# Kernel tuning notes

Measured on AMD Instinct MI355X. Metric: run time of the kernel, lower is better.

Reference implementation:

```python
import jax, jax.numpy as jnp
import numpy as np

N_NODES = 10000
N_EDGES = 64000
N_GRAPHS = 64
HID = 64


def _nnconv(h, src, dst, edge_attr, w1, b1, w2, b2, root, bias):
    # edge MLP: Linear(dim_edge,64) -> ReLU -> Linear(64, 64*64)
    we = (jax.nn.relu(edge_attr @ w1 + b1) @ w2 + b2).reshape(-1, HID, HID)  # [E,64,64]
    # per-edge matmul of gathered source features, then scatter-add to dst
    msg = jnp.einsum('ei,eio->eo', h[src], we)                               # [E,64]
    agg = jax.ops.segment_sum(msg, dst, num_segments=N_NODES)               # [N,64]
    return agg + h @ root + bias


def setup_inputs() -> dict:
    key = jax.random.key(0)
    ks = jax.random.split(key, 20)
    s = 0.05
    inp = {
        'x': jax.random.normal(ks[0], (N_NODES, 128), jnp.float32),
        'edge_index': jax.random.randint(ks[1], (2, N_EDGES), 0, N_NODES, dtype=jnp.int64),
        'edge_attr': jax.random.normal(ks[2], (N_EDGES, 32), jnp.float32),
        'batch': jnp.sort(jax.random.randint(ks[3], (N_NODES,), 0, N_GRAPHS, dtype=jnp.int64)),
        'nfc_w': jax.random.normal(ks[4], (128, HID), jnp.float32) * s,
        'nfc_b': jnp.zeros((HID,), jnp.float32),
        'efc1_w1': jax.random.normal(ks[5], (32, HID), jnp.float32) * s,
        'efc1_b1': jnp.zeros((HID,), jnp.float32),
        'efc1_w2': jax.random.normal(ks[6], (HID, HID * HID), jnp.float32) * s,
        'efc1_b2': jnp.zeros((HID * HID,), jnp.float32),
        'gc1_root': jax.random.normal(ks[7], (HID, HID), jnp.float32) * s,
        'gc1_bias': jnp.zeros((HID,), jnp.float32),
        'efc2_w1': jax.random.normal(ks[8], (32, HID), jnp.float32) * s,
        'efc2_b1': jnp.zeros((HID,), jnp.float32),
        'efc2_w2': jax.random.normal(ks[9], (HID, HID * HID), jnp.float32) * s,
        'efc2_b2': jnp.zeros((HID * HID,), jnp.float32),
        'gc2_root': jax.random.normal(ks[10], (HID, HID), jnp.float32) * s,
        'gc2_bias': jnp.zeros((HID,), jnp.float32),
        'fc1_w': jax.random.normal(ks[11], (HID, 32), jnp.float32) * s,
        'fc1_b': jnp.zeros((32,), jnp.float32),
        'fc2_w': jax.random.normal(ks[12], (32, 1), jnp.float32) * s,
        'fc2_b': jnp.zeros((1,), jnp.float32),
    }
    return inp


def reference(x, edge_index, edge_attr, batch,
              nfc_w, nfc_b,
              efc1_w1, efc1_b1, efc1_w2, efc1_b2, gc1_root, gc1_bias,
              efc2_w1, efc2_b1, efc2_w2, efc2_b2, gc2_root, gc2_bias,
              fc1_w, fc1_b, fc2_w, fc2_b):
    lrelu = lambda v: jax.nn.leaky_relu(v, 0.01)
    src, dst = edge_index[0], edge_index[1]
    hx = lrelu(x @ nfc_w + nfc_b)
    hx = lrelu(_nnconv(hx, src, dst, edge_attr, efc1_w1, efc1_b1, efc1_w2, efc1_b2, gc1_root, gc1_bias))
    hx = lrelu(_nnconv(hx, src, dst, edge_attr, efc2_w1, efc2_b1, efc2_w2, efc2_b2, gc2_root, gc2_bias))
    hg = jax.ops.segment_sum(hx, batch, num_segments=N_GRAPHS)  # global_add_pool -> [G,64]
    hg = lrelu(hg @ fc1_w + fc1_b)
    return hg @ fc2_w + fc2_b
```

## Files before the change

### kernel.cpp

```cpp
#include <hip/hip_runtime.h>
#include <hip/hip_bf16.h>

#define N_NODES  10000
#define N_EDGES  64000
#define N_GRAPHS 64
#define HID      64

typedef __attribute__((ext_vector_type(8))) short short8;
typedef __attribute__((ext_vector_type(4))) float f32x4;

__device__ __forceinline__ float lrelu(float v){ return v > 0.f ? v : 0.01f*v; }

__device__ __forceinline__ unsigned short f2bf(float f){
    union { float f; unsigned u; } v; v.f = f;
    unsigned r = v.u + 0x7fff + ((v.u >> 16) & 1);
    return (unsigned short)(r >> 16);
}
__device__ __forceinline__ float bf2f(unsigned short s){
    union { unsigned u; float f; } v; v.u = ((unsigned)s) << 16;
    return v.f;
}

#define PRE_NFC 2500
#define PRE_W2C 128
#define PRE_TR  4
#define PRE_CNT 250
__global__ void __launch_bounds__(256) pre_kernel(
        const float* __restrict__ x, const float* __restrict__ nfc_w, const float* __restrict__ nfc_b,
        float* __restrict__ hx1,
        const float* __restrict__ e1w2, unsigned short* __restrict__ w2t1,
        const float* __restrict__ e2w2, unsigned short* __restrict__ w2t2,
        const float* __restrict__ e1w1, unsigned short* __restrict__ w1t1,
        const float* __restrict__ e2w1, unsigned short* __restrict__ w1t2,
        const float* __restrict__ e1b2, unsigned short* __restrict__ b2t1,
        const float* __restrict__ e2b2, unsigned short* __restrict__ b2t2,
        const int* __restrict__ src, int* __restrict__ counts){
    __shared__ float tile[64][65];
    int b = blockIdx.x, tid = threadIdx.x;
    if (b < PRE_NFC){
        int m = tid & 63, n = b * 4 + (tid >> 6);
        float acc = nfc_b[m];
        const float* row = x + (size_t)n * 128;
        #pragma unroll 8
        for (int k = 0; k < 128; ++k) acc += row[k] * nfc_w[k * 64 + m];
        hx1[(size_t)n * 64 + m] = lrelu(acc);
    } else if (b < PRE_NFC + PRE_W2C){
        int bb = b - PRE_NFC;
        int k = bb & 63;
        const float* srcw = ((bb < 64) ? e1w2 : e2w2) + (size_t)k * 4096;
        unsigned short* dstw = (bb < 64) ? w2t1 : w2t2;
        for (int idx = tid; idx < 4096; idx += 256) tile[idx >> 6][idx & 63] = srcw[idx];
        __syncthreads();
        for (int idx = tid; idx < 4096; idx += 256){
            int o = idx >> 6, i = idx & 63;
            dstw[((size_t)(k * 64 + o) << 6) + i] = f2bf(tile[i][o]);
        }
    } else if (b < PRE_NFC + PRE_W2C + PRE_TR){
        int bb = b - PRE_NFC - PRE_W2C;
        if (bb < 2){
            const float* w1 = bb ? e2w1 : e1w1;
            unsigned short* w1t = bb ? w1t2 : w1t1;
            for (int idx = tid; idx < 2048; idx += 256){
                int o = idx >> 5, k = idx & 31;
                w1t[idx] = f2bf(w1[k * 64 + o]);
            }
        } else {
            const float* b2 = (bb == 3) ? e2b2 : e1b2;
            unsigned short* b2t = (bb == 3) ? b2t2 : b2t1;
            for (int idx = tid; idx < 4096; idx += 256){
                int o = idx >> 6, i = idx & 63;
                b2t[idx] = f2bf(b2[i * 64 + o]);
            }
        }
    } else {
        int e = (b - PRE_NFC - PRE_W2C - PRE_TR) * 256 + tid;
        if (e < N_EDGES) atomicAdd(&counts[src[e]], 1);
    }
}

__global__ void csr_scan_kernel(const int* __restrict__ counts, int* __restrict__ rowptr,
                                int* __restrict__ cursor){
    __shared__ int part[256];
    int tid = threadIdx.x;
    const int CH = (N_NODES + 255) / 256;
    int base = tid * CH, s = 0;
    for (int i = 0; i < CH; ++i){ int idx = base + i; if (idx < N_NODES){ cursor[idx] = 0; s += counts[idx]; } }
    part[tid] = s; __syncthreads();
    for (int off = 1; off < 256; off <<= 1){
        int v = (tid >= off) ? part[tid - off] : 0;
        __syncthreads();
        part[tid] += v;
        __syncthreads();
    }
    int run = part[tid] - s;
    for (int i = 0; i < CH; ++i){ int idx = base + i; if (idx < N_NODES){ rowptr[idx] = run; run += counts[idx]; } }
    if (tid == 255) rowptr[N_NODES] = run;
}

__global__ void csr_scatter_kernel(const int* __restrict__ src, const int* __restrict__ dst,
                                   const int* __restrict__ rowptr, int* __restrict__ cursor,
                                   int* __restrict__ eidx, int* __restrict__ dsts){
    int e = blockIdx.x * 256 + threadIdx.x;
    if (e >= N_EDGES) return;
    int s = src[e];
    int j = rowptr[s] + atomicAdd(&cursor[s], 1);
    eidx[j] = e; dsts[j] = dst[e];
}

#define NBT2 1000
#define NBH2 157
#define NBG  (157 * 8)
template<int L2FLAG>
__global__ void __launch_bounds__(256) layerA_kernel(
        const float* __restrict__ ea, const int* __restrict__ eidx,
        const unsigned short* __restrict__ w1t, const float* __restrict__ b1,
        unsigned short* __restrict__ tp,
        const float* __restrict__ hx, const unsigned short* __restrict__ b2t,
        float* __restrict__ hb2, float* __restrict__ agg,
        const unsigned short* __restrict__ w2t, unsigned short* __restrict__ G,
        float* __restrict__ hg){
    __shared__ unsigned short stg[64 * 256];
    int b = blockIdx.x, tid = threadIdx.x;
    int wid = tid >> 6, l = tid & 63;
    int m16 = l & 15, grp = l >> 4;

    if (b < NBT2){
        int j = b * 64 + wid * 16 + m16;
        const float* row = ea + (size_t)eidx[j] * 32 + grp * 8;
        float4 f0 = *(const float4*)(row);
        float4 f1 = *(const float4*)(row + 4);
        short8 ef;
        ef[0]=(short)f2bf(f0.x); ef[1]=(short)f2bf(f0.y); ef[2]=(short)f2bf(f0.z); ef[3]=(short)f2bf(f0.w);
        ef[4]=(short)f2bf(f1.x); ef[5]=(short)f2bf(f1.y); ef[6]=(short)f2bf(f1.z); ef[7]=(short)f2bf(f1.w);
        #pragma unroll
        for (int TB = 0; TB < 64; TB += 16){
            short8 wf = *(const short8*)(w1t + (TB + m16) * 32 + grp * 8);
            f32x4 acc = *(const f32x4*)(b1 + TB + grp * 4);
            acc = __builtin_amdgcn_mfma_f32_16x16x32_bf16(wf, ef, acc, 0, 0, 0);
            unsigned p0 = (unsigned)f2bf(fmaxf(acc[0], 0.f)) | ((unsigned)f2bf(fmaxf(acc[1], 0.f)) << 16);
            unsigned p1 = (unsigned)f2bf(fmaxf(acc[2], 0.f)) | ((unsigned)f2bf(fmaxf(acc[3], 0.f)) << 16);
            uint2 pk; pk.x = p0; pk.y = p1;
            *(uint2*)(tp + ((size_t)j << 6) + TB + grp * 4) = pk;
        }
    } else if (b < NBT2 + NBH2){
        int bb = b - NBT2;
        int node = bb * 64 + wid * 16 + m16;
        short8 h0 = {0,0,0,0,0,0,0,0}, h1 = {0,0,0,0,0,0,0,0};
        if (node < N_NODES){
            const float* hp = hx + ((size_t)node << 6) + grp * 8;
            float4 f0 = *(const float4*)(hp);
            float4 f1 = *(const float4*)(hp + 4);
            float4 f2 = *(const float4*)(hp + 32);
            float4 f3 = *(const float4*)(hp + 36);
            h0[0]=(short)f2bf(f0.x); h0[1]=(short)f2bf(f0.y); h0[2]=(short)f2bf(f0.z); h0[3]=(short)f2bf(f0.w);
            h0[4]=(short)f2bf(f1.x); h0[5]=(short)f2bf(f1.y); h0[6]=(short)f2bf(f1.z); h0[7]=(short)f2bf(f1.w);
            h1[0]=(short)f2bf(f2.x); h1[1]=(short)f2bf(f2.y); h1[2]=(short)f2bf(f2.z); h1[3]=(short)f2bf(f2.w);
            h1[4]=(short)f2bf(f3.x); h1[5]=(short)f2bf(f3.y); h1[6]=(short)f2bf(f3.z); h1[7]=(short)f2bf(f3.w);
        }
        #pragma unroll
        for (int TB = 0; TB < 64; TB += 16){
            short8 c0 = *(const short8*)(b2t + (TB + m16) * 64 + grp * 8);
            short8 c1 = *(const short8*)(b2t + (TB + m16) * 64 + 32 + grp * 8);
            f32x4 acc = {0.f, 0.f, 0.f, 0.f};
            acc = __builtin_amdgcn_mfma_f32_16x16x32_bf16(c0, h0, acc, 0, 0, 0);
            acc = __builtin_amdgcn_mfma_f32_16x16x32_bf16(c1, h1, acc, 0, 0, 0);
            if (node < N_NODES) *(f32x4*)(hb2 + ((size_t)node << 6) + TB + grp * 4) = acc;
        }
        f32x4 z = {0.f, 0.f, 0.f, 0.f};
        #pragma unroll
        for (int q = 0; q < 4; ++q){
            int chunk = q * 256 + tid;
            int n = bb * 64 + (chunk >> 4), c = (chunk & 15) * 4;
            if (n < N_NODES) *(f32x4*)(agg + ((size_t)n << 6) + c) = z;
        }
    } else if (b < NBT2 + NBH2 + NBG){
        int g = b - NBT2 - NBH2;
        int bx = g >> 3, by = g & 7;
        int n0 = bx * 64;
        int cb = by * 512;

        short8 bf0[4], bf1[4];
        #pragma unroll
        for (int ng = 0; ng < 4; ++ng){
            int node = n0 + ng * 16 + m16;
            short8 b0 = {0,0,0,0,0,0,0,0}, b1v = {0,0,0,0,0,0,0,0};
            if (node < N_NODES){
                const float* hp = hx + ((size_t)node << 6) + grp * 8;
                float4 f0 = *(const float4*)(hp);
                float4 f1 = *(const float4*)(hp + 4);
                float4 f2 = *(const float4*)(hp + 32);
                float4 f3 = *(const float4*)(hp + 36);
                b0[0]=(short)f2bf(f0.x); b0[1]=(short)f2bf(f0.y); b0[2]=(short)f2bf(f0.z); b0[3]=(short)f2bf(f0.w);
                b0[4]=(short)f2bf(f1.x); b0[5]=(short)f2bf(f1.y); b0[6]=(short)f2bf(f1.z); b0[7]=(short)f2bf(f1.w);
                b1v[0]=(short)f2bf(f2.x); b1v[1]=(short)f2bf(f2.y); b1v[2]=(short)f2bf(f2.z); b1v[3]=(short)f2bf(f2.w);
                b1v[4]=(short)f2bf(f3.x); b1v[5]=(short)f2bf(f3.y); b1v[6]=(short)f2bf(f3.z); b1v[7]=(short)f2bf(f3.w);
            }
            bf0[ng] = b0; bf1[ng] = b1v;
        }

        for (int h = 0; h < 2; ++h){
            #pragma unroll
            for (int tt = 0; tt < 4; ++tt){
                int t = h * 4 + tt;
                int TB = cb + t * 64 + wid * 16;
                const unsigned short* ap = w2t + ((size_t)(TB + m16) << 6) + grp * 8;
                short8 a0 = *(const short8*)ap;
                short8 a1 = *(const short8*)(ap + 32);
                int inrow = (tt * 128 + wid * 32 + grp * 8) ^ ((m16 & 7) << 4);
                #pragma unroll
                for (int ng = 0; ng < 4; ++ng){
                    f32x4 acc = {0.f, 0.f, 0.f, 0.f};
                    acc = __builtin_amdgcn_mfma_f32_16x16x32_bf16(a0, bf0[ng], acc, 0, 0, 0);
                    acc = __builtin_amdgcn_mfma_f32_16x16x32_bf16(a1, bf1[ng], acc, 0, 0, 0);
                    unsigned p0 = (unsigned)f2bf(acc[0]) | ((unsigned)f2bf(acc[1]) << 16);
                    unsigned p1 = (unsigned)f2bf(acc[2]) | ((unsigned)f2bf(acc[3]) << 16);
                    int row = ng * 16 + m16;
                    uint2 pk; pk.x = p0; pk.y = p1;
                    *(uint2*)((char*)stg + row * 512 + inrow) = pk;
                }
            }
            __syncthreads();
            #pragma unroll
            for (int s = 0; s < 8; ++s){
                int ci = s * 256 + tid;
                int row = ci >> 5;
                int node = n0 + row;
                uint4 v = *(uint4*)((char*)stg + row * 512 + (((ci & 31) * 16) ^ ((row & 7) << 4)));
                if (node < N_NODES)
                    *(uint4*)(G + ((size_t)node << 12) + cb + h * 256 + (ci & 31) * 8) = v;
            }
            __syncthreads();
        }
    } else if (L2FLAG){
        for (int i = tid; i < N_GRAPHS * 64; i += 256) hg[i] = 0.f;
    }
}

__global__ void __launch_bounds__(64) msg_csr_kernel(
        const unsigned short* __restrict__ tp, const unsigned short* __restrict__ G,
        const float* __restrict__ hb2, const int* __restrict__ rowptr,
        const int* __restrict__ dsts, float* __restrict__ agg){
    int s = blockIdx.x;
    int o = threadIdx.x;
    __shared__ unsigned short gl[4096];
    __shared__ unsigned short ts[64] __attribute__((aligned(16)));
    int r0 = rowptr[s], r1 = rowptr[s + 1];
    if (r0 == r1) return;
    const short8* gsrc = (const short8*)(G + ((size_t)s << 12));
    short8* gld = (short8*)gl;
    #pragma unroll
    for (int i = 0; i < 8; ++i) gld[i * 64 + o] = gsrc[i * 64 + o];
    float g[64];
    #pragma unroll
    for (int k = 0; k < 64; ++k) g[k] = bf2f(gl[k * 64 + o]);
    float hb = hb2[((size_t)s << 6) + o];
    for (int j = r0; j < r1; ++j){
        ts[o] = tp[((size_t)j << 6) + o];
        float acc = hb;
        #pragma unroll
        for (int k8 = 0; k8 < 8; ++k8){
            short8 tv = *(const short8*)&ts[k8 * 8];
            #pragma unroll
            for (int u = 0; u < 8; ++u) acc += bf2f((unsigned short)tv[u]) * g[k8 * 8 + u];
        }
        atomicAdd(&agg[((size_t)dsts[j] << 6) + o], acc);
    }
}

__global__ void combine_kernel(const float* __restrict__ agg, const float* __restrict__ hx,
                               const float* __restrict__ root, const float* __restrict__ bias,
                               float* __restrict__ out, int N){
    int m = threadIdx.x;
    int n = blockIdx.x * 4 + threadIdx.y;
    if (n >= N) return;
    float acc = agg[(size_t)n * 64 + m] + bias[m];
    const float* row = hx + (size_t)n * 64;
    #pragma unroll 8
    for (int k = 0; k < 64; ++k) acc += row[k] * root[k * 64 + m];
    out[(size_t)n * 64 + m] = lrelu(acc);
}

__global__ void combine2_kernel(const float* __restrict__ agg, const float* __restrict__ hx,
                                const float* __restrict__ root, const float* __restrict__ bias,
                                const int* __restrict__ batch, float* __restrict__ hg, int N){
    int m = threadIdx.x;
    int n = blockIdx.x * 4 + threadIdx.y;
    if (n >= N) return;
    float acc = agg[(size_t)n * 64 + m] + bias[m];
    const float* row = hx + (size_t)n * 64;
    #pragma unroll 8
    for (int k = 0; k < 64; ++k) acc += row[k] * root[k * 64 + m];
    atomicAdd(&hg[batch[n] * 64 + m], lrelu(acc));
}

__global__ void head_kernel(const float* __restrict__ hg, const float* __restrict__ fc1w,
                            const float* __restrict__ fc1b, const float* __restrict__ fc2w,
                            const float* __restrict__ fc2b, float* __restrict__ out){
    int g = threadIdx.x;
    const float* row = hg + g * 64;
    float h1[32];
    #pragma unroll
    for (int j = 0; j < 32; ++j){
        float a = fc1b[j];
        #pragma unroll 8
        for (int i = 0; i < 64; ++i) a += row[i] * fc1w[i * 32 + j];
        h1[j] = lrelu(a);
    }
    float o = fc2b[0];
    #pragma unroll
    for (int j = 0; j < 32; ++j) o += h1[j] * fc2w[j];
    out[g] = o;
}

extern "C" void kernel_launch(void* const* d_in, const int* in_sizes, int n_in,
                              void* d_out, int out_size, void* d_ws, size_t ws_size,
                              hipStream_t stream){
    const float* x      = (const float*)d_in[0];
    const int*   ei     = (const int*)  d_in[1];
    const float* ea     = (const float*)d_in[2];
    const int*   batch  = (const int*)  d_in[3];
    const float* nfc_w  = (const float*)d_in[4];
    const float* nfc_b  = (const float*)d_in[5];
    const float* e1w1   = (const float*)d_in[6];
    const float* e1b1   = (const float*)d_in[7];
    const float* e1w2   = (const float*)d_in[8];
    const float* e1b2   = (const float*)d_in[9];
    const float* g1root = (const float*)d_in[10];
    const float* g1bias = (const float*)d_in[11];
    const float* e2w1   = (const float*)d_in[12];
    const float* e2b1   = (const float*)d_in[13];
    const float* e2w2   = (const float*)d_in[14];
    const float* e2b2   = (const float*)d_in[15];
    const float* g2root = (const float*)d_in[16];
    const float* g2bias = (const float*)d_in[17];
    const float* fc1w   = (const float*)d_in[18];
    const float* fc1b   = (const float*)d_in[19];
    const float* fc2w   = (const float*)d_in[20];
    const float* fc2b   = (const float*)d_in[21];
    float* out = (float*)d_out;

    const int* src = ei;
    const int* dst = ei + N_EDGES;

    char* ws = (char*)d_ws;
    float* hx1 = (float*)ws;               ws += (size_t)N_NODES * 64 * 4;
    float* hx2 = (float*)ws;               ws += (size_t)N_NODES * 64 * 4;
    unsigned short* tp = (unsigned short*)ws; ws += (size_t)N_EDGES * 64 * 2;
    float* hb2 = (float*)ws;               ws += (size_t)N_NODES * 64 * 4;
    float* agg = (float*)ws;               ws += (size_t)N_NODES * 64 * 4;
    float* hg  = (float*)ws;               ws += (size_t)N_GRAPHS * 64 * 4;
    unsigned short* w2t1 = (unsigned short*)ws; ws += (size_t)64 * 64 * 64 * 2;
    unsigned short* w2t2 = (unsigned short*)ws; ws += (size_t)64 * 64 * 64 * 2;
    unsigned short* w1t1 = (unsigned short*)ws; ws += (size_t)2048 * 2;
    unsigned short* w1t2 = (unsigned short*)ws; ws += (size_t)2048 * 2;
    unsigned short* b2t1 = (unsigned short*)ws; ws += (size_t)4096 * 2;
    unsigned short* b2t2 = (unsigned short*)ws; ws += (size_t)4096 * 2;
    int* counts = (int*)ws;                ws += (size_t)10240 * 4;
    int* cursor = (int*)ws;                ws += (size_t)10240 * 4;
    int* rowptr = (int*)ws;                ws += (size_t)10240 * 4;
    int* eidx   = (int*)ws;                ws += (size_t)N_EDGES * 4;
    int* dsts   = (int*)ws;                ws += (size_t)N_EDGES * 4;
    unsigned short* G = (unsigned short*)ws;

    dim3 blk(64, 4);

    hipMemsetAsync(counts, 0, (size_t)N_NODES * 4, stream);
    pre_kernel<<<PRE_NFC + PRE_W2C + PRE_TR + PRE_CNT, 256, 0, stream>>>(
        x, nfc_w, nfc_b, hx1, e1w2, w2t1, e2w2, w2t2,
        e1w1, w1t1, e2w1, w1t2, e1b2, b2t1, e2b2, b2t2, src, counts);
    csr_scan_kernel<<<1, 256, 0, stream>>>(counts, rowptr, cursor);
    csr_scatter_kernel<<<N_EDGES / 256, 256, 0, stream>>>(src, dst, rowptr, cursor, eidx, dsts);

    layerA_kernel<0><<<NBT2 + NBH2 + NBG, 256, 0, stream>>>(
        ea, eidx, w1t1, e1b1, tp, hx1, b2t1, hb2, agg, w2t1, G, nullptr);
    msg_csr_kernel<<<N_NODES, 64, 0, stream>>>(tp, G, hb2, rowptr, dsts, agg);
    combine_kernel<<<N_NODES / 4, blk, 0, stream>>>(agg, hx1, g1root, g1bias, hx2, N_NODES);

    layerA_kernel<1><<<NBT2 + NBH2 + NBG + 1, 256, 0, stream>>>(
        ea, eidx, w1t2, e2b1, tp, hx2, b2t2, hb2, agg, w2t2, G, hg);
    msg_csr_kernel<<<N_NODES, 64, 0, stream>>>(tp, G, hb2, rowptr, dsts, agg);
    combine2_kernel<<<N_NODES / 4, blk, 0, stream>>>(agg, hx2, g2root, g2bias, batch, hg, N_NODES);

    head_kernel<<<1, 64, 0, stream>>>(hg, fc1w, fc1b, fc2w, fc2b, out);
}
```

Baseline: 254.2 us.

## Move edge-MLP first layer to pre-kernel and use MFMA for node linears

Both layers' edge MLP hidden activations (tp1, tp2) are now computed in the pre-kernel, in original edge order, from a single load of edge_attr. msg_csr reaches them through eidx. The input node linear and both root-combine linears now run on bf16 MFMA using pre-transposed bf16 weights produced by a new init kernel, which also replaces the memset. This aims to take the tp computation off the per-layer critical path and to cut scalar FMA work, at the cost of an extra tp buffer, an indirect gather in msg_csr, and bf16 rounding in the node and root matmuls.

```diff
diff --git a/kernel.cpp b/kernel.cpp
--- a/kernel.cpp
+++ b/kernel.cpp
@@ -20,32 +20,119 @@
     union { unsigned u; float f; } v; v.u = ((unsigned)s) << 16;
     return v.f;
 }
-
-#define PRE_NFC 2500
-#define PRE_W2C 128
-#define PRE_TR  4
-#define PRE_CNT 250
-__global__ void __launch_bounds__(256) pre_kernel(
-        const float* __restrict__ x, const float* __restrict__ nfc_w, const float* __restrict__ nfc_b,
-        float* __restrict__ hx1,
-        const float* __restrict__ e1w2, unsigned short* __restrict__ w2t1,
-        const float* __restrict__ e2w2, unsigned short* __restrict__ w2t2,
+__device__ __forceinline__ short8 pack_bf8(float4 a, float4 b){
+    short8 r;
+    r[0]=(short)f2bf(a.x); r[1]=(short)f2bf(a.y); r[2]=(short)f2bf(a.z); r[3]=(short)f2bf(a.w);
+    r[4]=(short)f2bf(b.x); r[5]=(short)f2bf(b.y); r[6]=(short)f2bf(b.z); r[7]=(short)f2bf(b.w);
+    return r;
+}
+
+__global__ void __launch_bounds__(256) init_kernel(
+        int* __restrict__ counts,
+        const float* __restrict__ nfc_w, unsigned short* __restrict__ nfc_wt,
         const float* __restrict__ e1w1, unsigned short* __restrict__ w1t1,
         const float* __restrict__ e2w1, unsigned short* __restrict__ w1t2,
         const float* __restrict__ e1b2, unsigned short* __restrict__ b2t1,
         const float* __restrict__ e2b2, unsigned short* __restrict__ b2t2,
+        const float* __restrict__ g1root, unsigned short* __restrict__ rootT1,
+        const float* __restrict__ g2root, unsigned short* __restrict__ rootT2){
+    int b = blockIdx.x, tid = threadIdx.x;
+    if (b < 40){
+        int i = b * 256 + tid;
+        if (i < N_NODES) counts[i] = 0;
+    } else if (b == 40){
+        for (int idx = tid; idx < 8192; idx += 256){
+            int o = idx >> 7, i = idx & 127;
+            nfc_wt[idx] = f2bf(nfc_w[i * 64 + o]);
+        }
+    } else if (b <= 42){
+        const float* w1 = (b == 42) ? e2w1 : e1w1;
+        unsigned short* w1t = (b == 42) ? w1t2 : w1t1;
+        for (int idx = tid; idx < 2048; idx += 256){
+            int o = idx >> 5, k = idx & 31;
+            w1t[idx] = f2bf(w1[k * 64 + o]);
+        }
+    } else if (b <= 44){
+        const float* b2 = (b == 44) ? e2b2 : e1b2;
+        unsigned short* b2t = (b == 44) ? b2t2 : b2t1;
+        for (int idx = tid; idx < 4096; idx += 256){
+            int o = idx >> 6, i = idx & 63;
+            b2t[idx] = f2bf(b2[i * 64 + o]);
+        }
+    } else {
+        const float* rt = (b == 46) ? g2root : g1root;
+        unsigned short* rT = (b == 46) ? rootT2 : rootT1;
+        for (int idx = tid; idx < 4096; idx += 256){
+            int o = idx >> 6, i = idx & 63;
+            rT[idx] = f2bf(rt[i * 64 + o]);
+        }
+    }
+}
+
+#define PRE_NFC 157
+#define PRE_TG  1000
+#define PRE_W2C 128
+#define PRE_CNT 250
+__global__ void __launch_bounds__(256) pre_kernel(
+        const float* __restrict__ x, const unsigned short* __restrict__ nfc_wt,
+        const float* __restrict__ nfc_b, float* __restrict__ hx1,
+        const float* __restrict__ ea,
+        const unsigned short* __restrict__ w1t1, const float* __restrict__ e1b1, unsigned short* __restrict__ tp1,
+        const unsigned short* __restrict__ w1t2, const float* __restrict__ e2b1, unsigned short* __restrict__ tp2,
+        const float* __restrict__ e1w2, unsigned short* __restrict__ w2t1,
+        const float* __restrict__ e2w2, unsigned short* __restrict__ w2t2,
         const int* __restrict__ src, int* __restrict__ counts){
     __shared__ float tile[64][65];
     int b = blockIdx.x, tid = threadIdx.x;
+    int wid = tid >> 6, l = tid & 63;
+    int m16 = l & 15, grp = l >> 4;
     if (b < PRE_NFC){
-        int m = tid & 63, n = b * 4 + (tid >> 6);
-        float acc = nfc_b[m];
-        const float* row = x + (size_t)n * 128;
-        #pragma unroll 8
-        for (int k = 0; k < 128; ++k) acc += row[k] * nfc_w[k * 64 + m];
-        hx1[(size_t)n * 64 + m] = lrelu(acc);
-    } else if (b < PRE_NFC + PRE_W2C){
-        int bb = b - PRE_NFC;
+        int node = b * 64 + wid * 16 + m16;
+        bool ok = node < N_NODES;
+        short8 xb[4];
+        #pragma unroll
+        for (int kq = 0; kq < 4; ++kq){
+            if (ok){
+                const float* xp = x + (size_t)node * 128 + kq * 32 + grp * 8;
+                xb[kq] = pack_bf8(*(const float4*)xp, *(const float4*)(xp + 4));
+            } else {
+                short8 z = {0,0,0,0,0,0,0,0}; xb[kq] = z;
+            }
+        }
+        #pragma unroll
+        for (int TB = 0; TB < 64; TB += 16){
+            f32x4 acc = *(const f32x4*)(nfc_b + TB + grp * 4);
+            #pragma unroll
+            for (int kq = 0; kq < 4; ++kq){
+                short8 af = *(const short8*)(nfc_wt + (TB + m16) * 128 + kq * 32 + grp * 8);
+                acc = __builtin_amdgcn_mfma_f32_16x16x32_bf16(af, xb[kq], acc, 0, 0, 0);
+            }
+            f32x4 r;
+            r[0] = lrelu(acc[0]); r[1] = lrelu(acc[1]); r[2] = lrelu(acc[2]); r[3] = lrelu(acc[3]);
+            if (ok) *(f32x4*)(hx1 + ((size_t)node << 6) + TB + grp * 4) = r;
+        }
+    } else if (b < PRE_NFC + PRE_TG){
+        int j = (b - PRE_NFC) * 64 + wid * 16 + m16;
+        const float* row = ea + (size_t)j * 32 + grp * 8;
+        short8 ef = pack_bf8(*(const float4*)row, *(const float4*)(row + 4));
+        #pragma unroll
+        for (int TB = 0; TB < 64; TB += 16){
+            short8 wf1 = *(const short8*)(w1t1 + (TB + m16) * 32 + grp * 8);
+            f32x4 a1 = *(const f32x4*)(e1b1 + TB + grp * 4);
+            a1 = __builtin_amdgcn_mfma_f32_16x16x32_bf16(wf1, ef, a1, 0, 0, 0);
+            uint2 p;
+            p.x = (unsigned)f2bf(fmaxf(a1[0], 0.f)) | ((unsigned)f2bf(fmaxf(a1[1], 0.f)) << 16);
+            p.y = (unsigned)f2bf(fmaxf(a1[2], 0.f)) | ((unsigned)f2bf(fmaxf(a1[3], 0.f)) << 16);
+            *(uint2*)(tp1 + ((size_t)j << 6) + TB + grp * 4) = p;
+            short8 wf2 = *(const short8*)(w1t2 + (TB + m16) * 32 + grp * 8);
+            f32x4 a2 = *(const f32x4*)(e2b1 + TB + grp * 4);
+            a2 = __builtin_amdgcn_mfma_f32_16x16x32_bf16(wf2, ef, a2, 0, 0, 0);
+            p.x = (unsigned)f2bf(fmaxf(a2[0], 0.f)) | ((unsigned)f2bf(fmaxf(a2[1], 0.f)) << 16);
+            p.y = (unsigned)f2bf(fmaxf(a2[2], 0.f)) | ((unsigned)f2bf(fmaxf(a2[3], 0.f)) << 16);
+            *(uint2*)(tp2 + ((size_t)j << 6) + TB + grp * 4) = p;
+        }
+    } else if (b < PRE_NFC + PRE_TG + PRE_W2C){
+        int bb = b - PRE_NFC - PRE_TG;
         int k = bb & 63;
         const float* srcw = ((bb < 64) ? e1w2 : e2w2) + (size_t)k * 4096;
         unsigned short* dstw = (bb < 64) ? w2t1 : w2t2;
@@ -55,25 +142,8 @@
             int o = idx >> 6, i = idx & 63;
             dstw[((size_t)(k * 64 + o) << 6) + i] = f2bf(tile[i][o]);
         }
-    } else if (b < PRE_NFC + PRE_W2C + PRE_TR){
-        int bb = b - PRE_NFC - PRE_W2C;
-        if (bb < 2){
-            const float* w1 = bb ? e2w1 : e1w1;
-            unsigned short* w1t = bb ? w1t2 : w1t1;
-            for (int idx = tid; idx < 2048; idx += 256){
-                int o = idx >> 5, k = idx & 31;
-                w1t[idx] = f2bf(w1[k * 64 + o]);
-            }
-        } else {
-            const float* b2 = (bb == 3) ? e2b2 : e1b2;
-            unsigned short* b2t = (bb == 3) ? b2t2 : b2t1;
-            for (int idx = tid; idx < 4096; idx += 256){
-                int o = idx >> 6, i = idx & 63;
-                b2t[idx] = f2bf(b2[i * 64 + o]);
-            }
-        }
     } else {
-        int e = (b - PRE_NFC - PRE_W2C - PRE_TR) * 256 + tid;
+        int e = (b - PRE_NFC - PRE_TG - PRE_W2C) * 256 + tid;
         if (e < N_EDGES) atomicAdd(&counts[src[e]], 1);
     }
 }
@@ -107,14 +177,10 @@
     eidx[j] = e; dsts[j] = dst[e];
 }
 
-#define NBT2 1000
 #define NBH2 157
 #define NBG  (157 * 8)
 template<int L2FLAG>
 __global__ void __launch_bounds__(256) layerA_kernel(
-        const float* __restrict__ ea, const int* __restrict__ eidx,
-        const unsigned short* __restrict__ w1t, const float* __restrict__ b1,
-        unsigned short* __restrict__ tp,
         const float* __restrict__ hx, const unsigned short* __restrict__ b2t,
         float* __restrict__ hb2, float* __restrict__ agg,
         const unsigned short* __restrict__ w2t, unsigned short* __restrict__ G,
@@ -124,38 +190,13 @@
     int wid = tid >> 6, l = tid & 63;
     int m16 = l & 15, grp = l >> 4;
 
-    if (b < NBT2){
-        int j = b * 64 + wid * 16 + m16;
-        const float* row = ea + (size_t)eidx[j] * 32 + grp * 8;
-        float4 f0 = *(const float4*)(row);
-        float4 f1 = *(const float4*)(row + 4);
-        short8 ef;
-        ef[0]=(short)f2bf(f0.x); ef[1]=(short)f2bf(f0.y); ef[2]=(short)f2bf(f0.z); ef[3]=(short)f2bf(f0.w);
-        ef[4]=(short)f2bf(f1.x); ef[5]=(short)f2bf(f1.y); ef[6]=(short)f2bf(f1.z); ef[7]=(short)f2bf(f1.w);
-        #pragma unroll
-        for (int TB = 0; TB < 64; TB += 16){
-            short8 wf = *(const short8*)(w1t + (TB + m16) * 32 + grp * 8);
-            f32x4 acc = *(const f32x4*)(b1 + TB + grp * 4);
-            acc = __builtin_amdgcn_mfma_f32_16x16x32_bf16(wf, ef, acc, 0, 0, 0);
-            unsigned p0 = (unsigned)f2bf(fmaxf(acc[0], 0.f)) | ((unsigned)f2bf(fmaxf(acc[1], 0.f)) << 16);
-            unsigned p1 = (unsigned)f2bf(fmaxf(acc[2], 0.f)) | ((unsigned)f2bf(fmaxf(acc[3], 0.f)) << 16);
-            uint2 pk; pk.x = p0; pk.y = p1;
-            *(uint2*)(tp + ((size_t)j << 6) + TB + grp * 4) = pk;
-        }
-    } else if (b < NBT2 + NBH2){
-        int bb = b - NBT2;
-        int node = bb * 64 + wid * 16 + m16;
+    if (b < NBH2){
+        int node = b * 64 + wid * 16 + m16;
         short8 h0 = {0,0,0,0,0,0,0,0}, h1 = {0,0,0,0,0,0,0,0};
         if (node < N_NODES){
             const float* hp = hx + ((size_t)node << 6) + grp * 8;
-            float4 f0 = *(const float4*)(hp);
-            float4 f1 = *(const float4*)(hp + 4);
-            float4 f2 = *(const float4*)(hp + 32);
-            float4 f3 = *(const float4*)(hp + 36);
-            h0[0]=(short)f2bf(f0.x); h0[1]=(short)f2bf(f0.y); h0[2]=(short)f2bf(f0.z); h0[3]=(short)f2bf(f0.w);
-            h0[4]=(short)f2bf(f1.x); h0[5]=(short)f2bf(f1.y); h0[6]=(short)f2bf(f1.z); h0[7]=(short)f2bf(f1.w);
-            h1[0]=(short)f2bf(f2.x); h1[1]=(short)f2bf(f2.y); h1[2]=(short)f2bf(f2.z); h1[3]=(short)f2bf(f2.w);
-            h1[4]=(short)f2bf(f3.x); h1[5]=(short)f2bf(f3.y); h1[6]=(short)f2bf(f3.z); h1[7]=(short)f2bf(f3.w);
+            h0 = pack_bf8(*(const float4*)hp, *(const float4*)(hp + 4));
+            h1 = pack_bf8(*(const float4*)(hp + 32), *(const float4*)(hp + 36));
         }
         #pragma unroll
         for (int TB = 0; TB < 64; TB += 16){
@@ -170,11 +211,11 @@
         #pragma unroll
         for (int q = 0; q < 4; ++q){
             int chunk = q * 256 + tid;
-            int n = bb * 64 + (chunk >> 4), c = (chunk & 15) * 4;
+            int n = b * 64 + (chunk >> 4), c = (chunk & 15) * 4;
             if (n < N_NODES) *(f32x4*)(agg + ((size_t)n << 6) + c) = z;
         }
-    } else if (b < NBT2 + NBH2 + NBG){
-        int g = b - NBT2 - NBH2;
+    } else if (b < NBH2 + NBG){
+        int g = b - NBH2;
         int bx = g >> 3, by = g & 7;
         int n0 = bx * 64;
         int cb = by * 512;
@@ -186,14 +227,8 @@
             short8 b0 = {0,0,0,0,0,0,0,0}, b1v = {0,0,0,0,0,0,0,0};
             if (node < N_NODES){
                 const float* hp = hx + ((size_t)node << 6) + grp * 8;
-                float4 f0 = *(const float4*)(hp);
-                float4 f1 = *(const float4*)(hp + 4);
-                float4 f2 = *(const float4*)(hp + 32);
-                float4 f3 = *(const float4*)(hp + 36);
-                b0[0]=(short)f2bf(f0.x); b0[1]=(short)f2bf(f0.y); b0[2]=(short)f2bf(f0.z); b0[3]=(short)f2bf(f0.w);
-                b0[4]=(short)f2bf(f1.x); b0[5]=(short)f2bf(f1.y); b0[6]=(short)f2bf(f1.z); b0[7]=(short)f2bf(f1.w);
-                b1v[0]=(short)f2bf(f2.x); b1v[1]=(short)f2bf(f2.y); b1v[2]=(short)f2bf(f2.z); b1v[3]=(short)f2bf(f2.w);
-                b1v[4]=(short)f2bf(f3.x); b1v[5]=(short)f2bf(f3.y); b1v[6]=(short)f2bf(f3.z); b1v[7]=(short)f2bf(f3.w);
+                b0  = pack_bf8(*(const float4*)hp, *(const float4*)(hp + 4));
+                b1v = pack_bf8(*(const float4*)(hp + 32), *(const float4*)(hp + 36));
             }
             bf0[ng] = b0; bf1[ng] = b1v;
         }
@@ -239,7 +274,8 @@
 __global__ void __launch_bounds__(64) msg_csr_kernel(
         const unsigned short* __restrict__ tp, const unsigned short* __restrict__ G,
         const float* __restrict__ hb2, const int* __restrict__ rowptr,
-        const int* __restrict__ dsts, float* __restrict__ agg){
+        const int* __restrict__ eidx, const int* __restrict__ dsts,
+        float* __restrict__ agg){
     int s = blockIdx.x;
     int o = threadIdx.x;
     __shared__ unsigned short gl[4096];
@@ -255,7 +291,8 @@
     for (int k = 0; k < 64; ++k) g[k] = bf2f(gl[k * 64 + o]);
     float hb = hb2[((size_t)s << 6) + o];
     for (int j = r0; j < r1; ++j){
-        ts[o] = tp[((size_t)j << 6) + o];
+        int e = eidx[j];
+        ts[o] = tp[((size_t)e << 6) + o];
         float acc = hb;
         #pragma unroll
         for (int k8 = 0; k8 < 8; ++k8){
@@ -267,30 +304,51 @@
     }
 }
 
-__global__ void combine_kernel(const float* __restrict__ agg, const float* __restrict__ hx,
-                               const float* __restrict__ root, const float* __restrict__ bias,
-                               float* __restrict__ out, int N){
-    int m = threadIdx.x;
-    int n = blockIdx.x * 4 + threadIdx.y;
-    if (n >= N) return;
-    float acc = agg[(size_t)n * 64 + m] + bias[m];
-    const float* row = hx + (size_t)n * 64;
-    #pragma unroll 8
-    for (int k = 0; k < 64; ++k) acc += row[k] * root[k * 64 + m];
-    out[(size_t)n * 64 + m] = lrelu(acc);
-}
-
-__global__ void combine2_kernel(const float* __restrict__ agg, const float* __restrict__ hx,
-                                const float* __restrict__ root, const float* __restrict__ bias,
-                                const int* __restrict__ batch, float* __restrict__ hg, int N){
-    int m = threadIdx.x;
-    int n = blockIdx.x * 4 + threadIdx.y;
-    if (n >= N) return;
-    float acc = agg[(size_t)n * 64 + m] + bias[m];
-    const float* row = hx + (size_t)n * 64;
-    #pragma unroll 8
-    for (int k = 0; k < 64; ++k) acc += row[k] * root[k * 64 + m];
-    atomicAdd(&hg[batch[n] * 64 + m], lrelu(acc));
+template<int L2>
+__global__ void __launch_bounds__(256) combine_kernel(
+        const float* __restrict__ agg, const float* __restrict__ hx,
+        const unsigned short* __restrict__ rootT, const float* __restrict__ bias,
+        float* __restrict__ outp, const int* __restrict__ batch, float* __restrict__ hg){
+    int b = blockIdx.x, tid = threadIdx.x;
+    int wid = tid >> 6, l = tid & 63;
+    int m16 = l & 15, grp = l >> 4;
+    int node = b * 64 + wid * 16 + m16;
+    bool ok = node < N_NODES;
+    short8 h0 = {0,0,0,0,0,0,0,0}, h1 = {0,0,0,0,0,0,0,0};
+    if (ok){
+        const float* hp = hx + ((size_t)node << 6) + grp * 8;
+        h0 = pack_bf8(*(const float4*)hp, *(const float4*)(hp + 4));
+        h1 = pack_bf8(*(const float4*)(hp + 32), *(const float4*)(hp + 36));
+    }
+    int bgi = ok ? batch[node] : 0;
+    #pragma unroll
+    for (int TB = 0; TB < 64; TB += 16){
+        short8 c0 = *(const short8*)(rootT + (TB + m16) * 64 + grp * 8);
+        short8 c1 = *(const short8*)(rootT + (TB + m16) * 64 + 32 + grp * 8);
+        f32x4 acc;
+        if (ok){
+            f32x4 av = *(const f32x4*)(agg + ((size_t)node << 6) + TB + grp * 4);
+            f32x4 bv = *(const f32x4*)(bias + TB + grp * 4);
+            acc[0] = av[0] + bv[0]; acc[1] = av[1] + bv[1];
+            acc[2] = av[2] + bv[2]; acc[3] = av[3] + bv[3];
+        } else {
+            acc[0] = acc[1] = acc[2] = acc[3] = 0.f;
+        }
+        acc = __builtin_amdgcn_mfma_f32_16x16x32_bf16(c0, h0, acc, 0, 0, 0);
+        acc = __builtin_amdgcn_mfma_f32_16x16x32_bf16(c1, h1, acc, 0, 0, 0);
+        if (ok){
+            if (L2){
+                #pragma unroll
+                for (int r = 0; r < 4; ++r)
+                    atomicAdd(&hg[bgi * 64 + TB + grp * 4 + r], lrelu(acc[r]));
+            } else {
+                f32x4 rv;
+                rv[0] = lrelu(acc[0]); rv[1] = lrelu(acc[1]);
+                rv[2] = lrelu(acc[2]); rv[3] = lrelu(acc[3]);
+                *(f32x4*)(outp + ((size_t)node << 6) + TB + grp * 4) = rv;
+            }
+        }
+    }
 }
 
 __global__ void head_kernel(const float* __restrict__ hg, const float* __restrict__ fc1w,
@@ -345,16 +403,20 @@
     char* ws = (char*)d_ws;
     float* hx1 = (float*)ws;               ws += (size_t)N_NODES * 64 * 4;
     float* hx2 = (float*)ws;               ws += (size_t)N_NODES * 64 * 4;
-    unsigned short* tp = (unsigned short*)ws; ws += (size_t)N_EDGES * 64 * 2;
+    unsigned short* tp1 = (unsigned short*)ws; ws += (size_t)N_EDGES * 64 * 2;
+    unsigned short* tp2 = (unsigned short*)ws; ws += (size_t)N_EDGES * 64 * 2;
     float* hb2 = (float*)ws;               ws += (size_t)N_NODES * 64 * 4;
     float* agg = (float*)ws;               ws += (size_t)N_NODES * 64 * 4;
     float* hg  = (float*)ws;               ws += (size_t)N_GRAPHS * 64 * 4;
     unsigned short* w2t1 = (unsigned short*)ws; ws += (size_t)64 * 64 * 64 * 2;
     unsigned short* w2t2 = (unsigned short*)ws; ws += (size_t)64 * 64 * 64 * 2;
+    unsigned short* nfc_wt = (unsigned short*)ws; ws += (size_t)8192 * 2;
     unsigned short* w1t1 = (unsigned short*)ws; ws += (size_t)2048 * 2;
     unsigned short* w1t2 = (unsigned short*)ws; ws += (size_t)2048 * 2;
     unsigned short* b2t1 = (unsigned short*)ws; ws += (size_t)4096 * 2;
     unsigned short* b2t2 = (unsigned short*)ws; ws += (size_t)4096 * 2;
+    unsigned short* rootT1 = (unsigned short*)ws; ws += (size_t)4096 * 2;
+    unsigned short* rootT2 = (unsigned short*)ws; ws += (size_t)4096 * 2;
     int* counts = (int*)ws;                ws += (size_t)10240 * 4;
     int* cursor = (int*)ws;                ws += (size_t)10240 * 4;
     int* rowptr = (int*)ws;                ws += (size_t)10240 * 4;
@@ -362,24 +424,21 @@
     int* dsts   = (int*)ws;                ws += (size_t)N_EDGES * 4;
     unsigned short* G = (unsigned short*)ws;
 
-    dim3 blk(64, 4);
-
-    hipMemsetAsync(counts, 0, (size_t)N_NODES * 4, stream);
-    pre_kernel<<<PRE_NFC + PRE_W2C + PRE_TR + PRE_CNT, 256, 0, stream>>>(
-        x, nfc_w, nfc_b, hx1, e1w2, w2t1, e2w2, w2t2,
-        e1w1, w1t1, e2w1, w1t2, e1b2, b2t1, e2b2, b2t2, src, counts);
+    init_kernel<<<47, 256, 0, stream>>>(counts, nfc_w, nfc_wt,
+        e1w1, w1t1, e2w1, w1t2, e1b2, b2t1, e2b2, b2t2, g1root, rootT1, g2root, rootT2);
+    pre_kernel<<<PRE_NFC + PRE_TG + PRE_W2C + PRE_CNT, 256, 0, stream>>>(
+        x, nfc_wt, nfc_b, hx1, ea, w1t1, e1b1, tp1, w1t2, e2b1, tp2,
+        e1w2, w2t1, e2w2, w2t2, src, counts);
     csr_scan_kernel<<<1, 256, 0, stream>>>(counts, rowptr, cursor);
     csr_scatter_kernel<<<N_EDGES / 256, 256, 0, stream>>>(src, dst, rowptr, cursor, eidx, dsts);
 
-    layerA_kernel<0><<<NBT2 + NBH2 + NBG, 256, 0, stream>>>(
-        ea, eidx, w1t1, e1b1, tp, hx1, b2t1, hb2, agg, w2t1, G, nullptr);
-    msg_csr_kernel<<<N_NODES, 64, 0, stream>>>(tp, G, hb2, rowptr, dsts, agg);
-    combine_kernel<<<N_NODES / 4, blk, 0, stream>>>(agg, hx1, g1root, g1bias, hx2, N_NODES);
-
-    layerA_kernel<1><<<NBT2 + NBH2 + NBG + 1, 256, 0, stream>>>(
-        ea, eidx, w1t2, e2b1, tp, hx2, b2t2, hb2, agg, w2t2, G, hg);
-    msg_csr_kernel<<<N_NODES, 64, 0, stream>>>(tp, G, hb2, rowptr, dsts, agg);
-    combine2_kernel<<<N_NODES / 4, blk, 0, stream>>>(agg, hx2, g2root, g2bias, batch, hg, N_NODES);
+    layerA_kernel<0><<<NBH2 + NBG, 256, 0, stream>>>(hx1, b2t1, hb2, agg, w2t1, G, nullptr);
+    msg_csr_kernel<<<N_NODES, 64, 0, stream>>>(tp1, G, hb2, rowptr, eidx, dsts, agg);
+    combine_kernel<0><<<157, 256, 0, stream>>>(agg, hx1, rootT1, g1bias, hx2, batch, nullptr);
+
+    layerA_kernel<1><<<NBH2 + NBG + 1, 256, 0, stream>>>(hx2, b2t2, hb2, agg, w2t2, G, hg);
+    msg_csr_kernel<<<N_NODES, 64, 0, stream>>>(tp2, G, hb2, rowptr, eidx, dsts, agg);
+    combine_kernel<1><<<157, 256, 0, stream>>>(agg, hx2, rootT2, g2bias, nullptr, batch, hg);
 
     head_kernel<<<1, 64, 0, stream>>>(hg, fc1w, fc1b, fc2w, fc2b, out);
 }
```

New measurement: 321.7 us. +26.6%, slower.
